# Kernel tuning notes

Hardware: AMD Instinct MI355X
Metric: run time of the kernel (lower is better)

## Reference

```python
import jax, jax.numpy as jnp
import numpy as np

B, S, D = 1, 2048, 1024
NH, HD, RD = 16, 64, 32        # nhead, head_dim, rope_dim (one head group)
KVC, QC = 256, 384             # kv / q compression dims
NSEQ = 4                       # len(tickers)
SPS = S // NSEQ                # seq_per_stock
LAMBDA_INIT = 0.8 - 0.6 * float(np.exp(-0.3 * 0))  # depth = 0 -> 0.2
EPS = 1e-5


def rmsnorm(x, w, eps=EPS):
    return x * jax.lax.rsqrt(jnp.mean(x * x, axis=-1, keepdims=True) + eps) * w


def setup_inputs() -> dict:
    key = jax.random.key(0)
    ks = jax.random.split(key, 12)
    w = lambda k, shape: jax.random.normal(k, shape, dtype=jnp.float32) * 0.02
    # causal mask, 1 (True) = masked; broadcast over head dim like torch masked_fill
    mask = jnp.triu(jnp.ones((S, S), dtype=bool), k=1)[None, None]
    # RoPE angles: dim = RD//2 = 16 half-dim rope features -> 8 complex freqs
    inv_freq = 1.0 / (10000.0 ** (np.arange(0, 16, 2, dtype=np.float32) / 16.0))
    freqs = jnp.asarray(np.outer(np.arange(SPS - 1, dtype=np.float32), inv_freq))
    return {
        "x": jax.random.normal(ks[0], (B, S, D), dtype=jnp.float32),
        "mask": mask,
        "freqs": freqs,
        "W_kv_down": w(ks[1], (D, KVC + RD)),
        "W_q_down": w(ks[2], (D, QC)),
        "kv_norm_w": jnp.ones((KVC,), jnp.float32),
        "q_norm_w": jnp.ones((QC,), jnp.float32),
        "W_kv_up": w(ks[3], (KVC, NH * HD * 2)),
        "W_q_up": w(ks[4], (QC, NH * (HD + RD))),
        "lambda_k1": jax.random.normal(ks[5], (HD // 2,), jnp.float32) * 0.1,
        "lambda_k2": jax.random.normal(ks[6], (HD // 2,), jnp.float32) * 0.1,
        "lambda_q1": jax.random.normal(ks[7], (HD // 2,), jnp.float32) * 0.1,
        "lambda_q2": jax.random.normal(ks[8], (HD // 2,), jnp.float32) * 0.1,
        "norm_w": jnp.ones((HD,), jnp.float32),
        "W_o": w(ks[9], (NH * HD, D)),
    }


def _rope_grouped(xr, freqs):
    # xr: [B, SPS, NSEQ, 2*NH, RD//2]; first token of each sub-sequence is kept
    # un-rotated (the 'separator'); remaining SPS-1 tokens get rotary embedding.
    head, rest = xr[:, :1], xr[:, 1:]
    r = rest.reshape(B, SPS - 1, NSEQ, 2 * NH, RD // 4, 2)
    cos = jnp.cos(freqs)[None, :, None, None, :]
    sin = jnp.sin(freqs)[None, :, None, None, :]
    a, b = r[..., 0], r[..., 1]
    rot = jnp.stack([a * cos - b * sin, a * sin + b * cos], axis=-1).reshape(rest.shape)
    return jnp.concatenate([head, rot], axis=1)


def reference(x, mask, freqs, W_kv_down, W_q_down, kv_norm_w, q_norm_w,
              W_kv_up, W_q_up, lambda_k1, lambda_k2, lambda_q1, lambda_q2,
              norm_w, W_o):
    # MLA down-projections + RMSNorm
    c = x @ W_kv_down                          # [B,S,KVC+RD]
    c_kv = rmsnorm(c[..., :KVC], kv_norm_w)
    k_rope_base = c[..., KVC:]                 # [B,S,RD]
    c_q = rmsnorm(x @ W_q_down, q_norm_w)

    # up-projections, split into paired half-dim heads (DINT)
    kv = (c_kv @ W_kv_up).reshape(B, S, NH, 2 * HD)
    k = kv[..., :HD].reshape(B, S, 2 * NH, HD // 2)
    v = kv[..., HD:]                           # [B,S,NH,HD]
    qp = (c_q @ W_q_up).reshape(B, S, NH, HD + RD)
    q = qp[..., :HD].reshape(B, S, 2 * NH, HD // 2)
    q_rope = qp[..., HD:].reshape(B, S, 2 * NH, RD // 2)
    k_rope = jnp.broadcast_to(k_rope_base[:, :, None, :], (B, S, NH, RD))
    k_rope = k_rope.reshape(B, S, 2 * NH, RD // 2)

    # per-sub-sequence RoPE (token t = p*NSEQ + s), vectorized over NSEQ
    q_rope = _rope_grouped(q_rope.reshape(B, SPS, NSEQ, 2 * NH, RD // 2), freqs)
    k_rope = _rope_grouped(k_rope.reshape(B, SPS, NSEQ, 2 * NH, RD // 2), freqs)
    q_rope = q_rope.reshape(B, S, 2 * NH, RD // 2)
    k_rope = k_rope.reshape(B, S, 2 * NH, RD // 2)

    q_f = jnp.concatenate([q, q_rope], -1).transpose(0, 2, 1, 3)  # [B,2NH,S,48]
    k_f = jnp.concatenate([k, k_rope], -1).transpose(0, 2, 1, 3)
    v_f = v.transpose(0, 2, 1, 3)                                 # [B,NH,S,HD]

    scale = ((HD + RD) // 2) ** (-0.5)
    a = jnp.einsum('bhqd,bhkd->bhqk', q_f, k_f) * scale
    abs_a = jnp.where(mask, -1e9, jnp.abs(a))
    a = jnp.sign(a) * jax.nn.softmax(abs_a, axis=-1)

    lam = (jnp.exp(jnp.sum(lambda_k1 * lambda_q1))
           - jnp.exp(jnp.sum(lambda_k2 * lambda_q2)) + LAMBDA_INIT)

    a = a.reshape(B, NH, 2, S, S)
    g = jnp.mean(a[:, :, 0], axis=-2, keepdims=True)   # [B,NH,1,S]
    a_final = a[:, :, 0] - lam * a[:, :, 1] + g * lam
    a_final = jnp.where(mask, 0.0, a_final)

    out = jnp.einsum('bhqk,bhkd->bhqd', a_final, v_f)  # [B,NH,S,HD]
    out = rmsnorm(out.transpose(0, 2, 1, 3), norm_w)   # [B,S,NH,HD]
    return out.reshape(B, S, NH * HD) @ W_o            # [B,S,D]
```

## Files before the change

kernel.cpp:

```cpp
#include <hip/hip_runtime.h>
#include <hip/hip_bf16.h>
#include <math.h>

constexpr int S    = 2048;
constexpr int D    = 1024;
constexpr int NH   = 16;
constexpr int H2   = 32;
constexpr int QKD  = 48;
constexpr int QKP  = 56;
constexpr int FCAP = 256;
constexpr float SCALE    = 0.14433756729740643f;
constexpr float LAM_INIT = 0.2f;
constexpr float EPS      = 1e-5f;
constexpr float THETA    = 1e-3f;

typedef __attribute__((ext_vector_type(8)))  short bf16x8;
typedef __attribute__((ext_vector_type(16))) float f32x16;

__device__ __forceinline__ int tile_order(int x) {
  return (x & 1) ? (31 - (x >> 1)) : (x >> 1);
}
__device__ __forceinline__ short f2bf(float x) {
  union { float f; unsigned u; } v; v.f = x;
  unsigned r = v.u + 0x7FFFu + ((v.u >> 16) & 1u);
  return (short)(r >> 16);
}
__device__ __forceinline__ float bf2f(short b) {
  union { unsigned u; float f; } v; v.u = ((unsigned)(unsigned short)b) << 16;
  return v.f;
}
__device__ __forceinline__ int d_rowpat(int r, int lane) {
  return (r & 3) + 8 * (r >> 2) + 4 * ((lane >> 5) & 1);
}
__device__ __forceinline__ f32x16 fzero16() {
  f32x16 z;
#pragma unroll
  for (int i = 0; i < 16; ++i) z[i] = 0.f;
  return z;
}
__device__ __forceinline__ bf16x8 frag56(const short* t, int lane, int sub, int ks) {
  return *(const bf16x8*)(t + ((lane & 31) + 32 * sub) * QKP + ((lane >> 5) << 3) + 16 * ks);
}
__device__ __forceinline__ bf16x8 frag72(const short* t, int lane, int sub, int ks) {
  return *(const bf16x8*)(t + ((lane & 31) + 32 * sub) * 72 + ((lane >> 5) << 3) + 16 * ks);
}
__device__ __forceinline__ f32x16 score_mfma(
    const short* ah, const short* al, const short* bh, const short* bl,
    int lane, int asub, int bsub) {
  f32x16 acc = fzero16();
#pragma unroll
  for (int t = 0; t < 3; ++t) {
    bf16x8 xh = frag56(ah, lane, asub, t);
    bf16x8 yh = frag56(bh, lane, bsub, t);
    bf16x8 xl = frag56(al, lane, asub, t);
    bf16x8 yl = frag56(bl, lane, bsub, t);
    acc = __builtin_amdgcn_mfma_f32_32x32x16_bf16(xh, yh, acc, 0, 0, 0);
    acc = __builtin_amdgcn_mfma_f32_32x32x16_bf16(xh, yl, acc, 0, 0, 0);
    acc = __builtin_amdgcn_mfma_f32_32x32x16_bf16(xl, yh, acc, 0, 0, 0);
  }
  return acc;
}
__device__ __forceinline__ f32x16 score_mfma1(
    const short* a, const short* b, int lane, int asub, int bsub) {
  f32x16 acc = fzero16();
#pragma unroll
  for (int t = 0; t < 3; ++t)
    acc = __builtin_amdgcn_mfma_f32_32x32x16_bf16(
        frag56(a, lane, asub, t), frag56(b, lane, bsub, t), acc, 0, 0, 0);
  return acc;
}
__device__ __forceinline__ void stage_tile(const unsigned* __restrict__ g,
                                           unsigned* __restrict__ lds, int tid) {
  for (int i = tid; i < 64 * 24; i += 256) {
    const int r = i / 24, c = i - r * 24;
    lds[r * 28 + c] = g[r * 24 + c];
  }
}
__device__ __forceinline__ void ldg_tile3(const unsigned* __restrict__ g,
                                          int tid, uint2 r[3]) {
  const uint2* g2 = (const uint2*)g;
#pragma unroll
  for (int j = 0; j < 3; ++j) r[j] = g2[tid + j * 256];
}
__device__ __forceinline__ void st_tile3(unsigned* __restrict__ lds,
                                         int tid, const uint2 r[3]) {
#pragma unroll
  for (int j = 0; j < 3; ++j) {
    const int e = 2 * (tid + j * 256);
    const int rr = e / 24, cc = e - rr * 24;
    *(uint2*)&lds[rr * 28 + cc] = r[j];
  }
}
__device__ __forceinline__ void ldg_t64(const unsigned* __restrict__ g,
                                        int ld_u2, int tid, uint2 r[4]) {
  const uint2* g2 = (const uint2*)g;
#pragma unroll
  for (int j = 0; j < 4; ++j) {
    const int e = tid + j * 256;
    const int row = e >> 4, c4 = e & 15;
    r[j] = g2[(size_t)row * ld_u2 + c4];
  }
}
__device__ __forceinline__ void st_t64(short* __restrict__ lds,
                                       int tid, const uint2 r[4]) {
#pragma unroll
  for (int j = 0; j < 4; ++j) {
    const int e = tid + j * 256;
    const int row = e >> 4, c4 = e & 15;
    *(uint2*)&lds[row * 72 + c4 * 4] = r[j];
  }
}
__device__ __forceinline__ void ldg_v4(const short* __restrict__ vb,
                                       int lane, int sub, int k0, bf16x8 r[4]) {
  const short* base = vb + ((size_t)((lane & 31) + 32 * sub)) * S + k0 +
                      ((lane >> 5) << 3);
#pragma unroll
  for (int t = 0; t < 4; ++t) r[t] = *(const bf16x8*)(base + 16 * t);
}
__device__ __forceinline__ float signedp(float sv, float mrow, float rrow) {
  const float e = __expf(fabsf(sv) - mrow) * rrow;
  return (sv > 0.f) ? e : ((sv < 0.f) ? -e : 0.f);
}
__device__ __forceinline__ float dot48(const float* __restrict__ a,
                                       const float* __restrict__ b) {
  float s = 0.f;
#pragma unroll
  for (int j = 0; j < 12; ++j) {
    float4 x = *(const float4*)&a[4 * j];
    float4 y = *(const float4*)&b[4 * j];
    s += x.x * y.x + x.y * y.y + x.z * y.z + x.w * y.w;
  }
  return s;
}

__global__ __launch_bounds__(256) void gemm_f32(
    const float* __restrict__ A, const float* __restrict__ B,
    float* __restrict__ C, int M, int K, int N) {
  __shared__ float As[16][64];
  __shared__ float Bs[16][128];
  const int tid = threadIdx.x;
  const int m0 = blockIdx.y * 64, n0 = blockIdx.x * 128;
  const int ty = tid >> 4, tx = tid & 15;
  float acc[4][8] = {};
  for (int k0 = 0; k0 < K; k0 += 16) {
    {
      const int am = tid >> 2;
      const int ak = (tid & 3) * 4;
      float4 a4 = *(const float4*)&A[(size_t)(m0 + am) * K + k0 + ak];
      As[ak + 0][am] = a4.x; As[ak + 1][am] = a4.y;
      As[ak + 2][am] = a4.z; As[ak + 3][am] = a4.w;
    }
#pragma unroll
    for (int it = 0; it < 2; ++it) {
      const int bk = (tid >> 5) + it * 8;
      const int bn = (tid & 31) * 4;
      const int gn = n0 + bn;
      float4 b4 = make_float4(0.f, 0.f, 0.f, 0.f);
      if (gn < N) b4 = *(const float4*)&B[(size_t)(k0 + bk) * N + gn];
      *(float4*)&Bs[bk][bn] = b4;
    }
    __syncthreads();
#pragma unroll
    for (int kk = 0; kk < 16; ++kk) {
      float a[4], b[8];
      *(float4*)&a[0] = *(const float4*)&As[kk][ty * 4];
      *(float4*)&b[0] = *(const float4*)&Bs[kk][tx * 8];
      *(float4*)&b[4] = *(const float4*)&Bs[kk][tx * 8 + 4];
#pragma unroll
      for (int r = 0; r < 4; ++r)
#pragma unroll
        for (int c = 0; c < 8; ++c) acc[r][c] += a[r] * b[c];
    }
    __syncthreads();
  }
#pragma unroll
  for (int r = 0; r < 4; ++r) {
    const int gm = m0 + ty * 4 + r;
#pragma unroll
    for (int c4 = 0; c4 < 2; ++c4) {
      const int gn = n0 + tx * 8 + c4 * 4;
      if (gn < N) {
        float4 v = make_float4(acc[r][c4 * 4], acc[r][c4 * 4 + 1],
                               acc[r][c4 * 4 + 2], acc[r][c4 * 4 + 3]);
        *(float4*)&C[(size_t)gm * N + gn] = v;
      }
    }
  }
}

__global__ __launch_bounds__(256) void rmsnorm_rows(
    const float* __restrict__ in, const float* __restrict__ w,
    float* __restrict__ out, int stride_in, int width) {
  const int row = blockIdx.x;
  const float* x = in + (size_t)row * stride_in;
  float ss = 0.f;
  for (int j = threadIdx.x; j < width; j += 256) { float v = x[j]; ss += v * v; }
  __shared__ float red[256];
  red[threadIdx.x] = ss;
  __syncthreads();
  for (int o = 128; o; o >>= 1) {
    if (threadIdx.x < o) red[threadIdx.x] += red[threadIdx.x + o];
    __syncthreads();
  }
  const float sc = rsqrtf(red[0] / (float)width + EPS);
  for (int j = threadIdx.x; j < width; j += 256)
    out[(size_t)row * width + j] = x[j] * sc * w[j];
}

__global__ __launch_bounds__(64) void assemble_qk(
    const float* __restrict__ qp, const float* __restrict__ kv,
    const float* __restrict__ c, const float* __restrict__ freqs,
    float* __restrict__ qfR, float* __restrict__ kfR,
    short* __restrict__ qhi, short* __restrict__ qlo,
    short* __restrict__ khi, short* __restrict__ klo) {
  const int h2 = blockIdx.x, s0 = blockIdx.y * 64;
  const int tid = threadIdx.x, s = s0 + tid;
  const int m = h2 >> 1, e = h2 & 1;
  const int sp = s >> 2;
  float cs[8], sn[8];
  if (sp > 0) {
#pragma unroll
    for (int t = 0; t < 8; ++t) {
      float a = freqs[(sp - 1) * 8 + t];
      cs[t] = cosf(a); sn[t] = sinf(a);
    }
  }
  float v[48], rr[16];
  {
    const float* qrow = qp + (size_t)s * (NH * 96) + m * 96;
#pragma unroll
    for (int j = 0; j < 32; ++j) v[j] = qrow[e * 32 + j];
#pragma unroll
    for (int j = 0; j < 16; ++j) rr[j] = qrow[64 + e * 16 + j];
    if (sp > 0) {
#pragma unroll
      for (int t = 0; t < 8; ++t) {
        float a = rr[2 * t], b = rr[2 * t + 1];
        rr[2 * t]     = a * cs[t] - b * sn[t];
        rr[2 * t + 1] = a * sn[t] + b * cs[t];
      }
    }
#pragma unroll
    for (int j = 0; j < 16; ++j) v[32 + j] = rr[j];
    float* dst = qfR + ((size_t)h2 * S + s) * 48;
#pragma unroll
    for (int j = 0; j < 12; ++j)
      *(float4*)&dst[4 * j] = make_float4(v[4 * j], v[4 * j + 1], v[4 * j + 2], v[4 * j + 3]);
    unsigned* dh = (unsigned*)(qhi + ((size_t)h2 * S + s) * 48);
    unsigned* dl = (unsigned*)(qlo + ((size_t)h2 * S + s) * 48);
#pragma unroll
    for (int j = 0; j < 24; ++j) {
      const short h0 = f2bf(v[2 * j]),     h1 = f2bf(v[2 * j + 1]);
      const short l0 = f2bf(v[2 * j] - bf2f(h0));
      const short l1 = f2bf(v[2 * j + 1] - bf2f(h1));
      dh[j] = (unsigned)(unsigned short)h0 | ((unsigned)(unsigned short)h1 << 16);
      dl[j] = (unsigned)(unsigned short)l0 | ((unsigned)(unsigned short)l1 << 16);
    }
  }
  {
    const float* krow = kv + (size_t)s * (NH * 128) + m * 128;
#pragma unroll
    for (int j = 0; j < 32; ++j) v[j] = krow[e * 32 + j];
#pragma unroll
    for (int j = 0; j < 16; ++j) rr[j] = c[(size_t)s * 288 + 256 + e * 16 + j];
    if (sp > 0) {
#pragma unroll
      for (int t = 0; t < 8; ++t) {
        float a = rr[2 * t], b = rr[2 * t + 1];
        rr[2 * t]     = a * cs[t] - b * sn[t];
        rr[2 * t + 1] = a * sn[t] + b * cs[t];
      }
    }
#pragma unroll
    for (int j = 0; j < 16; ++j) v[32 + j] = rr[j];
    float* dst = kfR + ((size_t)h2 * S + s) * 48;
#pragma unroll
    for (int j = 0; j < 12; ++j)
      *(float4*)&dst[4 * j] = make_float4(v[4 * j], v[4 * j + 1], v[4 * j + 2], v[4 * j + 3]);
    unsigned* dh = (unsigned*)(khi + ((size_t)h2 * S + s) * 48);
    unsigned* dl = (unsigned*)(klo + ((size_t)h2 * S + s) * 48);
#pragma unroll
    for (int j = 0; j < 24; ++j) {
      const short h0 = f2bf(v[2 * j]),     h1 = f2bf(v[2 * j + 1]);
      const short l0 = f2bf(v[2 * j] - bf2f(h0));
      const short l1 = f2bf(v[2 * j + 1] - bf2f(h1));
      dh[j] = (unsigned)(unsigned short)h0 | ((unsigned)(unsigned short)h1 << 16);
      dl[j] = (unsigned)(unsigned short)l0 | ((unsigned)(unsigned short)l1 << 16);
    }
  }
}

__global__ __launch_bounds__(256) void assemble_v(
    const float* __restrict__ kv, short* __restrict__ vThi,
    short* __restrict__ vTlo) {
  const int h = blockIdx.x, s0 = blockIdx.y * 64;
  const int tid = threadIdx.x;
  __shared__ float t[64][65];
  for (int i = tid; i < 4096; i += 256) {
    const int sl = i >> 6, dd = i & 63;
    t[sl][dd] = kv[(size_t)(s0 + sl) * (NH * 128) + h * 128 + 64 + dd];
  }
  __syncthreads();
  for (int i = tid; i < 4096; i += 256) {
    const int dd = i >> 6, sl = i & 63;
    const float v = t[sl][dd];
    const short hi = f2bf(v);
    vThi[((size_t)(h * 64 + dd)) * S + s0 + sl] = hi;
    vTlo[((size_t)(h * 64 + dd)) * S + s0 + sl] = f2bf(v - bf2f(hi));
  }
}

__global__ __launch_bounds__(256) void cvt_wo(
    const float* __restrict__ Wo, short* __restrict__ WoThi,
    short* __restrict__ WoTlo) {
  const int k0 = blockIdx.x * 64, n0 = blockIdx.y * 64;
  __shared__ float t[64][65];
  const int tid = threadIdx.x;
  for (int i = tid; i < 4096; i += 256) {
    const int kk = i >> 6, nn = i & 63;
    t[kk][nn] = Wo[(size_t)(k0 + kk) * D + n0 + nn];
  }
  __syncthreads();
  for (int i = tid; i < 4096; i += 256) {
    const int nn = i >> 6, kk = i & 63;
    const float v = t[kk][nn];
    const short hi = f2bf(v);
    WoThi[(size_t)(n0 + nn) * D + k0 + kk] = hi;
    WoTlo[(size_t)(n0 + nn) * D + k0 + kk] = f2bf(v - bf2f(hi));
  }
}

__global__ __launch_bounds__(64) void compute_lam(
    const float* __restrict__ lk1, const float* __restrict__ lk2,
    const float* __restrict__ lq1, const float* __restrict__ lq2,
    float* __restrict__ lam) {
  const int t = threadIdx.x;
  float p1 = (t < 32) ? lk1[t] * lq1[t] : 0.f;
  float p2 = (t < 32) ? lk2[t] * lq2[t] : 0.f;
  for (int o = 16; o; o >>= 1) {
    p1 += __shfl_down(p1, o);
    p2 += __shfl_down(p2, o);
  }
  if (t == 0) *lam = expf(p1) - expf(p2) + LAM_INIT;
}

__global__ __launch_bounds__(256) void attn_md(
    const short* __restrict__ qhi, const short* __restrict__ khi,
    float* __restrict__ mOut, float* __restrict__ rdOut) {
  const int tile = tile_order(blockIdx.x), h2 = blockIdx.y;
  const int q0 = tile * 64;
  __shared__ __align__(16) short qh_s[64 * QKP];
  __shared__ __align__(16) short kh_s[64 * QKP];
  __shared__ float mpart[2][64], dpart[2][64];
  const int tid = threadIdx.x, lane = tid & 63, w = tid >> 6;
  const int asub = w >> 1, bsub = w & 1;
  stage_tile((const unsigned*)(qhi + ((size_t)h2 * S + q0) * 48), (unsigned*)qh_s, tid);
  uint2 kh_r[3];
  ldg_tile3((const unsigned*)(khi + (size_t)h2 * S * 48), tid, kh_r);
  float m_acc = -1e30f, d_acc = 0.f;
  const int qg = q0 + 32 * bsub + (lane & 31);
  for (int kt = 0; kt <= tile; ++kt) {
    const int k0 = kt * 64;
    st_tile3((unsigned*)kh_s, tid, kh_r);
    if (kt < tile)
      ldg_tile3((const unsigned*)(khi + ((size_t)h2 * S + k0 + 64) * 48), tid, kh_r);
    __syncthreads();
    f32x16 acc = score_mfma1(kh_s, qh_s, lane, asub, bsub);
    float av[16];
    float tm = -1e30f;
    if (kt < tile) {
#pragma unroll
      for (int r = 0; r < 16; ++r) { av[r] = fabsf(acc[r] * SCALE); tm = fmaxf(tm, av[r]); }
    } else {
#pragma unroll
      for (int r = 0; r < 16; ++r) {
        const int kg = k0 + 32 * asub + d_rowpat(r, lane);
        av[r] = (kg <= qg) ? fabsf(acc[r] * SCALE) : -1e30f;
        tm = fmaxf(tm, av[r]);
      }
    }
    const float nm = fmaxf(m_acc, tm);
    if (nm > -1e29f) {
      float add = 0.f;
#pragma unroll
      for (int r = 0; r < 16; ++r) add += __expf(av[r] - nm);
      d_acc = d_acc * __expf(m_acc - nm) + add;
      m_acc = nm;
    }
    __syncthreads();
  }
  {
    const float m2 = __shfl_xor(m_acc, 32);
    const float d2 = __shfl_xor(d_acc, 32);
    const float nm = fmaxf(m_acc, m2);
    float dd = 0.f;
    if (nm > -1e29f) dd = d_acc * __expf(m_acc - nm) + d2 * __expf(m2 - nm);
    if ((lane & 32) == 0) {
      mpart[asub][32 * bsub + (lane & 31)] = nm;
      dpart[asub][32 * bsub + (lane & 31)] = dd;
    }
  }
  __syncthreads();
  if (tid < 64) {
    const float ma = mpart[0][tid], mb = mpart[1][tid];
    const float da = dpart[0][tid], db = dpart[1][tid];
    const float mm = fmaxf(ma, mb);
    const float dsum = da * __expf(ma - mm) + db * __expf(mb - mm);
    mOut[h2 * S + q0 + tid] = mm;
    rdOut[h2 * S + q0 + tid] = 1.0f / dsum;
  }
}

__global__ __launch_bounds__(256) void attn_outp(
    const short* __restrict__ qhi, const short* __restrict__ qlo,
    const short* __restrict__ khi, const short* __restrict__ klo,
    const float* __restrict__ qfR, const float* __restrict__ kfR,
    const short* __restrict__ vThi, const short* __restrict__ vTlo,
    const float* __restrict__ mIn, const float* __restrict__ rdIn,
    float* __restrict__ opA0, float* __restrict__ opB0,
    float* __restrict__ opA1, float* __restrict__ opB1,
    float* __restrict__ gp) {
  const int tile = tile_order(blockIdx.x), h2 = blockIdx.y;
  const int chunk = blockIdx.z;
  const int h = h2 >> 1;
  const int q0 = tile * 64;
  __shared__ __align__(16) short qh_s[64 * QKP], ql_s[64 * QKP];
  __shared__ __align__(16) short kh_s[64 * QKP], kl_s[64 * QKP];
  __shared__ __align__(16) short ph_s[64 * 72], pl_s[64 * 72];
  __shared__ float mrow[64], rrow[64];
  __shared__ float gcol[2][64];
  __shared__ int fixq[FCAP];
  __shared__ int fixcnt;
  const int tid = threadIdx.x, lane = tid & 63, w = tid >> 6;
  const int qsub = w >> 1, sub2 = w & 1;
  const short* vbh = vThi + ((size_t)h * 64) * S;
  const short* vbl = vTlo + ((size_t)h * 64) * S;
  const float* qf = qfR + (size_t)h2 * S * 48;
  const float* kf = kfR + (size_t)h2 * S * 48;
  stage_tile((const unsigned*)(qhi + ((size_t)h2 * S + q0) * 48), (unsigned*)qh_s, tid);
  stage_tile((const unsigned*)(qlo + ((size_t)h2 * S + q0) * 48), (unsigned*)ql_s, tid);
  if (tid < 64) {
    mrow[tid] = mIn[h2 * S + q0 + tid];
    rrow[tid] = rdIn[h2 * S + q0 + tid];
  }
  uint2 kh_r[3], kl_r[3];
  bf16x8 vh_r[4], vl_r[4];
  const int kstart = (chunk <= tile) ? chunk : tile;
  ldg_tile3((const unsigned*)(khi + ((size_t)h2 * S + kstart * 64) * 48), tid, kh_r);
  ldg_tile3((const unsigned*)(klo + ((size_t)h2 * S + kstart * 64) * 48), tid, kl_r);
  ldg_v4(vbh, lane, sub2, kstart * 64, vh_r);
  ldg_v4(vbl, lane, sub2, kstart * 64, vl_r);
  f32x16 oacc = fzero16();
  const int colk = 32 * sub2 + (lane & 31);
  for (int kt = chunk; kt <= tile; kt += 2) {
    const int k0 = kt * 64;
    st_tile3((unsigned*)kh_s, tid, kh_r);
    st_tile3((unsigned*)kl_s, tid, kl_r);
    if (tid == 0) fixcnt = 0;
    if (kt + 2 <= tile) {
      ldg_tile3((const unsigned*)(khi + ((size_t)h2 * S + k0 + 128) * 48), tid, kh_r);
      ldg_tile3((const unsigned*)(klo + ((size_t)h2 * S + k0 + 128) * 48), tid, kl_r);
    }
    __syncthreads();
    f32x16 a = score_mfma(qh_s, ql_s, kh_s, kl_s, lane, qsub, sub2);
    const bool dg = (kt == tile);
    const int kg = k0 + colk;
    float colsum = 0.f;
#pragma unroll
    for (int r = 0; r < 16; ++r) {
      const int row = d_rowpat(r, lane) + 32 * qsub;
      float p = 0.f;
      if (!dg || kg <= (q0 + row)) {
        const float s = a[r];
        p = signedp(s * SCALE, mrow[row], rrow[row]);
        if (fabsf(s) < THETA) {
          const int sg = (s > 0.f) ? 1 : ((s < 0.f) ? 2 : 0);
          const int slot = atomicAdd(&fixcnt, 1);
          if (slot < FCAP) fixq[slot] = (row << 8) | (colk << 2) | sg;
        }
      }
      colsum += p;
      const short ph = f2bf(p);
      ph_s[row * 72 + colk] = ph;
      pl_s[row * 72 + colk] = f2bf(p - bf2f(ph));
    }
    colsum += __shfl_xor(colsum, 32);
    if ((lane & 32) == 0) gcol[qsub][colk] = colsum;
    __syncthreads();
    if ((h2 & 1) == 0 && tid < 64)
      gp[((size_t)(tile * NH + h)) * S + k0 + tid] = gcol[0][tid] + gcol[1][tid];
    if (fixcnt > 0) {
      const int cnt = min(fixcnt, FCAP);
#pragma unroll 1
      for (int i = tid; i < cnt; i += 256) {
        const int e = fixq[i];
        const int row = (e >> 8) & 63, ck = (e >> 2) & 63, sgc = e & 3;
        const float sgo = (sgc == 1) ? 1.f : ((sgc == 2) ? -1.f : 0.f);
        const float sx = dot48(qf + (size_t)(q0 + row) * 48,
                               kf + (size_t)(k0 + ck) * 48);
        const float sgn = (sx > 0.f) ? 1.f : ((sx < 0.f) ? -1.f : 0.f);
        if (sgn != sgo) {
          const float delta = (sgn - sgo) * __expf(-mrow[row]) * rrow[row];
          const int off = row * 72 + ck;
          const float pv = bf2f(ph_s[off]) + bf2f(pl_s[off]) + delta;
          const short nh = f2bf(pv);
          ph_s[off] = nh;
          pl_s[off] = f2bf(pv - bf2f(nh));
        }
      }
      __syncthreads();
    }
#pragma unroll
    for (int t = 0; t < 4; ++t) {
      bf16x8 pa = frag72(ph_s, lane, qsub, t);
      bf16x8 pl = frag72(pl_s, lane, qsub, t);
      oacc = __builtin_amdgcn_mfma_f32_32x32x16_bf16(pa, vh_r[t], oacc, 0, 0, 0);
      oacc = __builtin_amdgcn_mfma_f32_32x32x16_bf16(pa, vl_r[t], oacc, 0, 0, 0);
      oacc = __builtin_amdgcn_mfma_f32_32x32x16_bf16(pl, vh_r[t], oacc, 0, 0, 0);
    }
    if (kt + 2 <= tile) {
      ldg_v4(vbh, lane, sub2, k0 + 128, vh_r);
      ldg_v4(vbl, lane, sub2, k0 + 128, vl_r);
    }
  }
  float* op = (h2 & 1) ? (chunk ? opB1 : opB0) : (chunk ? opA1 : opA0);
#pragma unroll
  for (int r = 0; r < 16; ++r) {
    const int row = d_rowpat(r, lane) + 32 * qsub;
    op[((size_t)h * S + q0 + row) * 64 + colk] = oacc[r];
  }
}

__global__ __launch_bounds__(256) void g_reduce(
    const float* __restrict__ gp, float* __restrict__ g) {
  const int k = blockIdx.x * 256 + threadIdx.x;
  const int h = blockIdx.y;
  const int kt = k >> 6;
  float s = 0.f;
  for (int qt = kt; qt < 32; ++qt) s += gp[((size_t)(qt * NH + h)) * S + k];
  g[h * S + k] = s * (1.0f / (float)S);
}

__global__ __launch_bounds__(64) void gvc_scan1(
    const float* __restrict__ g, const short* __restrict__ vThi,
    const short* __restrict__ vTlo, float* __restrict__ gvc,
    float* __restrict__ csum) {
  const int chunk = blockIdx.x, h = blockIdx.y, dd = threadIdx.x;
  const int k0 = chunk * 64;
  const short* vh = vThi + ((size_t)(h * 64 + dd)) * S + k0;
  const short* vl = vTlo + ((size_t)(h * 64 + dd)) * S + k0;
  const float* gr = g + h * S + k0;
  float run = 0.f;
#pragma unroll 8
  for (int k = 0; k < 64; ++k) {
    run += gr[k] * (bf2f(vh[k]) + bf2f(vl[k]));
    gvc[((size_t)(h * S + k0 + k)) * 64 + dd] = run;
  }
  csum[((size_t)h * 32 + chunk) * 64 + dd] = run;
}
__global__ __launch_bounds__(64) void gvc_scan2(
    float* __restrict__ gvc, const float* __restrict__ csum) {
  const int chunk = blockIdx.x + 1, h = blockIdx.y, dd = threadIdx.x;
  float off = 0.f;
  for (int j = 0; j < chunk; ++j) off += csum[((size_t)h * 32 + j) * 64 + dd];
  const int k0 = chunk * 64;
#pragma unroll 8
  for (int k = 0; k < 64; ++k)
    gvc[((size_t)(h * S + k0 + k)) * 64 + dd] += off;
}

__global__ __launch_bounds__(256) void combine_out(
    const float* __restrict__ opA0, const float* __restrict__ opA1,
    const float* __restrict__ opB0, const float* __restrict__ opB1,
    const float* __restrict__ gvc, const float* __restrict__ lamPtr,
    const float* __restrict__ normW,
    short* __restrict__ nhi, short* __restrict__ nlo) {
  const int h = blockIdx.y, q0 = blockIdx.x * 64;
  const int tid = threadIdx.x, d = tid & 63, wv = tid >> 6;
  const float lam = *lamPtr;
  const float wn = normW[d];
#pragma unroll 4
  for (int i = 0; i < 16; ++i) {
    const int q = q0 + wv + 4 * i;
    const size_t off = ((size_t)h * S + q) * 64 + d;
    float val = (opA0[off] + opA1[off]) - lam * (opB0[off] + opB1[off])
              + lam * gvc[off];
    float ss = val * val;
#pragma unroll
    for (int o = 1; o < 64; o <<= 1) ss += __shfl_xor(ss, o);
    const float sc = rsqrtf(ss * (1.0f / 64.0f) + EPS);
    const float ov = val * sc * wn;
    const short hi = f2bf(ov);
    nhi[(size_t)q * D + h * 64 + d] = hi;
    nlo[(size_t)q * D + h * 64 + d] = f2bf(ov - bf2f(hi));
  }
}

__global__ __launch_bounds__(256) void gemm_bf16s(
    const short* __restrict__ Ahi, const short* __restrict__ Alo,
    const short* __restrict__ BThi, const short* __restrict__ BTlo,
    float* __restrict__ C) {
  const int n0 = blockIdx.x * 64, m0 = blockIdx.y * 64;
  __shared__ __align__(16) short ah_s[64 * 72], al_s[64 * 72];
  __shared__ __align__(16) short bh_s[64 * 72], bl_s[64 * 72];
  const int tid = threadIdx.x, lane = tid & 63, w = tid >> 6;
  const int msub = w >> 1, nsub = w & 1;
  uint2 ah_r[4], al_r[4], bh_r[4], bl_r[4];
  ldg_t64((const unsigned*)(Ahi + (size_t)m0 * D), 256, tid, ah_r);
  ldg_t64((const unsigned*)(Alo + (size_t)m0 * D), 256, tid, al_r);
  ldg_t64((const unsigned*)(BThi + (size_t)n0 * D), 256, tid, bh_r);
  ldg_t64((const unsigned*)(BTlo + (size_t)n0 * D), 256, tid, bl_r);
  f32x16 acc = fzero16();
  for (int kc = 0; kc < 16; ++kc) {
    st_t64(ah_s, tid, ah_r); st_t64(al_s, tid, al_r);
    st_t64(bh_s, tid, bh_r); st_t64(bl_s, tid, bl_r);
    if (kc < 15) {
      const int k0 = (kc + 1) * 64;
      ldg_t64((const unsigned*)(Ahi + (size_t)m0 * D + k0), 256, tid, ah_r);
      ldg_t64((const unsigned*)(Alo + (size_t)m0 * D + k0), 256, tid, al_r);
      ldg_t64((const unsigned*)(BThi + (size_t)n0 * D + k0), 256, tid, bh_r);
      ldg_t64((const unsigned*)(BTlo + (size_t)n0 * D + k0), 256, tid, bl_r);
    }
    __syncthreads();
#pragma unroll
    for (int t = 0; t < 4; ++t) {
      bf16x8 xh = frag72(ah_s, lane, msub, t);
      bf16x8 xl = frag72(al_s, lane, msub, t);
      bf16x8 yh = frag72(bh_s, lane, nsub, t);
      bf16x8 yl = frag72(bl_s, lane, nsub, t);
      acc = __builtin_amdgcn_mfma_f32_32x32x16_bf16(xh, yh, acc, 0, 0, 0);
      acc = __builtin_amdgcn_mfma_f32_32x32x16_bf16(xh, yl, acc, 0, 0, 0);
      acc = __builtin_amdgcn_mfma_f32_32x32x16_bf16(xl, yh, acc, 0, 0, 0);
    }
    __syncthreads();
  }
  const int col = 32 * nsub + (lane & 31);
#pragma unroll
  for (int r = 0; r < 16; ++r) {
    const int row = d_rowpat(r, lane) + 32 * msub;
    C[(size_t)(m0 + row) * D + n0 + col] = acc[r];
  }
}

extern "C" void kernel_launch(void* const* d_in, const int* in_sizes, int n_in,
                              void* d_out, int out_size, void* d_ws, size_t ws_size,
                              hipStream_t stream) {
  const float* x     = (const float*)d_in[0];
  const float* freqs = (const float*)d_in[2];
  const float* Wkvd  = (const float*)d_in[3];
  const float* Wqd   = (const float*)d_in[4];
  const float* kvnw  = (const float*)d_in[5];
  const float* qnw   = (const float*)d_in[6];
  const float* Wkvup = (const float*)d_in[7];
  const float* Wqup  = (const float*)d_in[8];
  const float* lk1   = (const float*)d_in[9];
  const float* lk2   = (const float*)d_in[10];
  const float* lq1   = (const float*)d_in[11];
  const float* lq2   = (const float*)d_in[12];
  const float* normw = (const float*)d_in[13];
  const float* Wo    = (const float*)d_in[14];
  float* out = (float*)d_out;

  float* ws = (float*)d_ws;
  float* c      = ws;
  float* ckv    = c     + (size_t)S * 288;
  float* cqr    = ckv   + (size_t)S * 256;
  float* cq     = cqr   + (size_t)S * 384;
  float* kvbuf  = cq    + (size_t)S * 384;
  float* qp     = kvbuf + (size_t)S * 2048;
  float* qfR    = qp    + (size_t)S * 1536;
  float* kfR    = qfR   + (size_t)H2 * S * 48;
  short* qhi    = (short*)(kfR + (size_t)H2 * S * 48);
  short* qlo    = qhi + (size_t)H2 * S * 48;
  short* khi    = qlo + (size_t)H2 * S * 48;
  short* klo    = khi + (size_t)H2 * S * 48;
  short* vThi   = klo + (size_t)H2 * S * 48;
  short* vTlo   = vThi + (size_t)NH * 64 * S;
  float* mbuf   = (float*)(vTlo + (size_t)NH * 64 * S);
  float* rdbuf  = mbuf  + (size_t)H2 * S;
  float* gbuf   = rdbuf + (size_t)H2 * S;
  float* lam    = gbuf  + (size_t)NH * S;
  float* csum   = lam + 1;
  float* opB1   = csum + (size_t)NH * 32 * 64;
  short* nhi    = (short*)(opB1 + (size_t)NH * S * 64);
  short* nlo    = nhi + (size_t)S * D;
  short* WoThi  = nlo + (size_t)S * D;
  short* WoTlo  = WoThi + (size_t)D * D;
  float* gvc    = kvbuf;
  float* opB0   = kvbuf + (size_t)NH * S * 64;
  float* opA0   = ckv;
  float* opA1   = qp;
  float* gp     = qp + (size_t)NH * S * 64;

  cvt_wo<<<dim3(16, 16), 256, 0, stream>>>(Wo, WoThi, WoTlo);
  gemm_f32<<<dim3(3, S / 64), 256, 0, stream>>>(x, Wkvd, c, S, D, 288);
  gemm_f32<<<dim3(3, S / 64), 256, 0, stream>>>(x, Wqd, cqr, S, D, 384);
  rmsnorm_rows<<<S, 256, 0, stream>>>(c, kvnw, ckv, 288, 256);
  rmsnorm_rows<<<S, 256, 0, stream>>>(cqr, qnw, cq, 384, 384);
  gemm_f32<<<dim3(16, S / 64), 256, 0, stream>>>(ckv, Wkvup, kvbuf, S, 256, 2048);
  gemm_f32<<<dim3(12, S / 64), 256, 0, stream>>>(cq, Wqup, qp, S, 384, 1536);
  assemble_qk<<<dim3(H2, S / 64), 64, 0, stream>>>(qp, kvbuf, c, freqs,
                                                   qfR, kfR, qhi, qlo, khi, klo);
  assemble_v<<<dim3(NH, S / 64), 256, 0, stream>>>(kvbuf, vThi, vTlo);
  compute_lam<<<1, 64, 0, stream>>>(lk1, lk2, lq1, lq2, lam);
  attn_md<<<dim3(32, H2), 256, 0, stream>>>(qhi, khi, mbuf, rdbuf);
  attn_outp<<<dim3(32, H2, 2), 256, 0, stream>>>(qhi, qlo, khi, klo, qfR, kfR,
                                                 vThi, vTlo, mbuf, rdbuf,
                                                 opA0, opB0, opA1, opB1, gp);
  g_reduce<<<dim3(S / 256, NH), 256, 0, stream>>>(gp, gbuf);
  gvc_scan1<<<dim3(32, NH), 64, 0, stream>>>(gbuf, vThi, vTlo, gvc, csum);
  gvc_scan2<<<dim3(31, NH), 64, 0, stream>>>(gvc, csum);
  combine_out<<<dim3(S / 64, NH), 256, 0, stream>>>(opA0, opA1, opB0, opB1,
                                                    gvc, lam, normw, nhi, nlo);
  gemm_bf16s<<<dim3(D / 64, S / 64), 256, 0, stream>>>(nhi, nlo, WoThi, WoTlo, out);
}
```

Baseline: 778.8 us.

## Double-buffer K tile in attn_md and apply sign fixes directly to output accumulators

attn_md now double-buffers the K tile in shared memory, so the trailing barrier in each loop iteration can be removed. In attn_outp the near-zero-score sign correction no longer patches the P tile in shared memory behind an extra barrier. Instead, after the PV MFMAs each lane rescans the fix list and adds delta*V straight into its own output accumulator register. The fix list is double-buffered by iteration parity and its capacity is halved. The trade-offs are redundant per-lane list scans, scalar global V reads, and a higher chance of overflowing the smaller list.

```diff
diff --git a/kernel.cpp b/kernel.cpp
--- a/kernel.cpp
+++ b/kernel.cpp
@@ -8,7 +8,7 @@
 constexpr int H2   = 32;
 constexpr int QKD  = 48;
 constexpr int QKP  = 56;
-constexpr int FCAP = 256;
+constexpr int FCAP = 128;
 constexpr float SCALE    = 0.14433756729740643f;
 constexpr float LAM_INIT = 0.2f;
 constexpr float EPS      = 1e-5f;
@@ -350,7 +350,7 @@
   const int tile = tile_order(blockIdx.x), h2 = blockIdx.y;
   const int q0 = tile * 64;
   __shared__ __align__(16) short qh_s[64 * QKP];
-  __shared__ __align__(16) short kh_s[64 * QKP];
+  __shared__ __align__(16) short kh_s[2][64 * QKP];
   __shared__ float mpart[2][64], dpart[2][64];
   const int tid = threadIdx.x, lane = tid & 63, w = tid >> 6;
   const int asub = w >> 1, bsub = w & 1;
@@ -361,11 +361,12 @@
   const int qg = q0 + 32 * bsub + (lane & 31);
   for (int kt = 0; kt <= tile; ++kt) {
     const int k0 = kt * 64;
-    st_tile3((unsigned*)kh_s, tid, kh_r);
+    short* kb = kh_s[kt & 1];
+    st_tile3((unsigned*)kb, tid, kh_r);
     if (kt < tile)
       ldg_tile3((const unsigned*)(khi + ((size_t)h2 * S + k0 + 64) * 48), tid, kh_r);
     __syncthreads();
-    f32x16 acc = score_mfma1(kh_s, qh_s, lane, asub, bsub);
+    f32x16 acc = score_mfma1(kb, qh_s, lane, asub, bsub);
     float av[16];
     float tm = -1e30f;
     if (kt < tile) {
@@ -387,7 +388,6 @@
       d_acc = d_acc * __expf(m_acc - nm) + add;
       m_acc = nm;
     }
-    __syncthreads();
   }
   {
     const float m2 = __shfl_xor(m_acc, 32);
@@ -429,8 +429,8 @@
   __shared__ __align__(16) short ph_s[64 * 72], pl_s[64 * 72];
   __shared__ float mrow[64], rrow[64];
   __shared__ float gcol[2][64];
-  __shared__ int fixq[FCAP];
-  __shared__ int fixcnt;
+  __shared__ int fixq[2][FCAP];
+  __shared__ int fixcnt[2];
   const int tid = threadIdx.x, lane = tid & 63, w = tid >> 6;
   const int qsub = w >> 1, sub2 = w & 1;
   const short* vbh = vThi + ((size_t)h * 64) * S;
@@ -454,9 +454,10 @@
   const int colk = 32 * sub2 + (lane & 31);
   for (int kt = chunk; kt <= tile; kt += 2) {
     const int k0 = kt * 64;
+    const int par = ((kt - chunk) >> 1) & 1;
     st_tile3((unsigned*)kh_s, tid, kh_r);
     st_tile3((unsigned*)kl_s, tid, kl_r);
-    if (tid == 0) fixcnt = 0;
+    if (tid == 0) fixcnt[par] = 0;
     if (kt + 2 <= tile) {
       ldg_tile3((const unsigned*)(khi + ((size_t)h2 * S + k0 + 128) * 48), tid, kh_r);
       ldg_tile3((const unsigned*)(klo + ((size_t)h2 * S + k0 + 128) * 48), tid, kl_r);
@@ -475,8 +476,8 @@
         p = signedp(s * SCALE, mrow[row], rrow[row]);
         if (fabsf(s) < THETA) {
           const int sg = (s > 0.f) ? 1 : ((s < 0.f) ? 2 : 0);
-          const int slot = atomicAdd(&fixcnt, 1);
-          if (slot < FCAP) fixq[slot] = (row << 8) | (colk << 2) | sg;
+          const int slot = atomicAdd(&fixcnt[par], 1);
+          if (slot < FCAP) fixq[par][slot] = (row << 8) | (colk << 2) | sg;
         }
       }
       colsum += p;
@@ -487,29 +488,9 @@
     colsum += __shfl_xor(colsum, 32);
     if ((lane & 32) == 0) gcol[qsub][colk] = colsum;
     __syncthreads();
+    const int cnt = min(fixcnt[par], FCAP);
     if ((h2 & 1) == 0 && tid < 64)
       gp[((size_t)(tile * NH + h)) * S + k0 + tid] = gcol[0][tid] + gcol[1][tid];
-    if (fixcnt > 0) {
-      const int cnt = min(fixcnt, FCAP);
-#pragma unroll 1
-      for (int i = tid; i < cnt; i += 256) {
-        const int e = fixq[i];
-        const int row = (e >> 8) & 63, ck = (e >> 2) & 63, sgc = e & 3;
-        const float sgo = (sgc == 1) ? 1.f : ((sgc == 2) ? -1.f : 0.f);
-        const float sx = dot48(qf + (size_t)(q0 + row) * 48,
-                               kf + (size_t)(k0 + ck) * 48);
-        const float sgn = (sx > 0.f) ? 1.f : ((sx < 0.f) ? -1.f : 0.f);
-        if (sgn != sgo) {
-          const float delta = (sgn - sgo) * __expf(-mrow[row]) * rrow[row];
-          const int off = row * 72 + ck;
-          const float pv = bf2f(ph_s[off]) + bf2f(pl_s[off]) + delta;
-          const short nh = f2bf(pv);
-          ph_s[off] = nh;
-          pl_s[off] = f2bf(pv - bf2f(nh));
-        }
-      }
-      __syncthreads();
-    }
 #pragma unroll
     for (int t = 0; t < 4; ++t) {
       bf16x8 pa = frag72(ph_s, lane, qsub, t);
@@ -517,6 +498,26 @@
       oacc = __builtin_amdgcn_mfma_f32_32x32x16_bf16(pa, vh_r[t], oacc, 0, 0, 0);
       oacc = __builtin_amdgcn_mfma_f32_32x32x16_bf16(pa, vl_r[t], oacc, 0, 0, 0);
       oacc = __builtin_amdgcn_mfma_f32_32x32x16_bf16(pl, vh_r[t], oacc, 0, 0, 0);
+    }
+#pragma unroll 1
+    for (int i = 0; i < cnt; ++i) {
+      const int e = fixq[par][i];
+      const int row = (e >> 8) & 63, ck = (e >> 2) & 63, sgc = e & 3;
+      if ((row >> 5) != qsub) continue;
+      if (((lane >> 5) & 1) != ((row >> 2) & 1)) continue;
+      const float sgo = (sgc == 1) ? 1.f : ((sgc == 2) ? -1.f : 0.f);
+      const float sx = dot48(qf + (size_t)(q0 + row) * 48,
+                             kf + (size_t)(k0 + ck) * 48);
+      const float sgn = (sx > 0.f) ? 1.f : ((sx < 0.f) ? -1.f : 0.f);
+      if (sgn != sgo) {
+        const float delta = (sgn - sgo) * __expf(-mrow[row]) * rrow[row];
+        const float v = bf2f(vbh[(size_t)colk * S + k0 + ck]) +
+                        bf2f(vbl[(size_t)colk * S + k0 + ck]);
+        const float dv = delta * v;
+        const int rr = (((row & 31) >> 3) << 2) | (row & 3);
+#pragma unroll
+        for (int r = 0; r < 16; ++r) if (r == rr) oacc[r] += dv;
+      }
     }
     if (kt + 2 <= tile) {
       ldg_v4(vbh, lane, sub2, k0 + 128, vh_r);
```

Measured after the change: 842.9 us. +8.2%, slower.
